# Kernel optimization log

Measured on AMD Instinct MI355X. Metric: run time of the kernel, lower is better.

## Reference

```python
import jax, jax.numpy as jnp
import numpy as np
import math

B, S, E, H, DFF = 4, 1024, 1024, 16, 4096
HD = E // H
EPS = 1e-8


def setup_inputs() -> dict:
    key = jax.random.key(0)
    ks = jax.random.split(key, 16)
    sc = 0.02
    inp = {
        'x': jax.random.normal(ks[0], (B, S, E), jnp.float32),
        'mask': jax.random.randint(ks[1], (B, S, S), 0, 2, jnp.int32),
        'Wq': jax.random.normal(ks[2], (E, E), jnp.float32) * sc,
        'bq': jnp.zeros((E,), jnp.float32),
        'Wk': jax.random.normal(ks[3], (E, E), jnp.float32) * sc,
        'bk': jnp.zeros((E,), jnp.float32),
        'Wv': jax.random.normal(ks[4], (E, E), jnp.float32) * sc,
        'bv': jnp.zeros((E,), jnp.float32),
        'Wo': jax.random.normal(ks[5], (E, E), jnp.float32) * sc,
        'bo': jnp.zeros((E,), jnp.float32),
        'W1': jax.random.normal(ks[6], (DFF, E), jnp.float32) * sc,
        'b1': jnp.zeros((DFF,), jnp.float32),
        'W2': jax.random.normal(ks[7], (E, DFF), jnp.float32) * sc,
        'b2': jnp.zeros((E,), jnp.float32),
        'g1': jnp.ones((E,), jnp.float32),
        'be1': jnp.zeros((E,), jnp.float32),
        'g2': jnp.ones((E,), jnp.float32),
        'be2': jnp.zeros((E,), jnp.float32),
    }
    return inp


def _layernorm(x, g, b):
    # torch LayerNorm here: (x-mean)/(std+eps), std is unbiased (ddof=1)
    mean = jnp.mean(x, axis=-1, keepdims=True)
    std = jnp.std(x, axis=-1, keepdims=True, ddof=1)
    return g * (x - mean) / (std + EPS) + b


def _gelu(x):
    c = math.sqrt(2.0 / math.pi)
    return 0.5 * x * (1.0 + jnp.tanh(c * (x + 0.044715 * x ** 3)))


def _block(x, mask_f, Wq, bq, Wk, bk, Wv, bv, Wo, bo, W1, b1, W2, b2, g1, be1, g2, be2):
    # --- attention sublayer (pre-norm, residual) ---
    nx = _layernorm(x, g1, be1)
    q = (nx @ Wq.T + bq).reshape(B, S, H, HD).transpose(0, 2, 1, 3)  # [B,H,S,D]
    k = (nx @ Wk.T + bk).reshape(B, S, H, HD).transpose(0, 2, 1, 3)
    v = (nx @ Wv.T + bv).reshape(B, S, H, HD).transpose(0, 2, 1, 3)
    scores = jnp.einsum('bhqd,bhkd->bhqk', q, k) / math.sqrt(HD)
    m = mask_f[:, None, :, :]  # [B,1,S,S]
    scores = jnp.where(m == 0, jnp.float32(-0.01), scores * m)
    p = jax.nn.softmax(scores, axis=-1)
    o = jnp.einsum('bhqk,bhkd->bhqd', p, v)  # [B,H,S,D]
    o = o.transpose(0, 2, 1, 3).reshape(B, S, E)
    x = x + (o @ Wo.T + bo)
    # --- FFN sublayer ---
    nx2 = _layernorm(x, g2, be2)
    ff = _gelu(nx2 @ W1.T + b1) @ W2.T + b2
    return x + ff


def reference(x, mask, Wq, bq, Wk, bk, Wv, bv, Wo, bo, W1, b1, W2, b2, g1, be1, g2, be2):
    mask_f = mask.astype(jnp.float32)
    return _block(x, mask_f, Wq, bq, Wk, bk, Wv, bv, Wo, bo, W1, b1, W2, b2, g1, be1, g2, be2)
```

## Files before the change

### kernel.cpp

```cpp
#include <hip/hip_runtime.h>
#include <math.h>

typedef __attribute__((ext_vector_type(8))) short short8;
typedef __attribute__((ext_vector_type(4))) float f32x4;
typedef __attribute__((ext_vector_type(4))) int   i32x4v;

#define B_   4
#define S_   1024
#define E_   1024
#define H_   16
#define DFF_ 4096

#define HB_MAX 4.0f

__device__ __forceinline__ ushort f2bf(float f){
  unsigned int x = __float_as_uint(f);
  x += 0x7fffu + ((x >> 16) & 1u);
  return (ushort)(x >> 16);
}

__device__ __forceinline__ unsigned int pk_bf16_trunc(float a, float b){
  return __builtin_amdgcn_perm(__float_as_uint(b), __float_as_uint(a), 0x07060302u);
}

__device__ __forceinline__ float gelu_f(float x){
  const float c = 0.7978845608028654f;
  float u = 2.0f * c * (x + 0.044715f * x * x * x);
  return x / (1.0f + __expf(-u));
}

__device__ __forceinline__ void gl2lds16(const void* g, void* l){
  __builtin_amdgcn_global_load_lds(
      (const __attribute__((address_space(1))) void*)g,
      (__attribute__((address_space(3))) void*)l, 16, 0, 0);
}

__device__ __forceinline__ int q8(float x, float s){
  float v = fmaxf(fminf(x * s, 127.f), -127.f);
  return ((int)__builtin_rintf(v)) & 255;
}
__device__ __forceinline__ int pk_i8x4(float a, float b, float c, float d, float s){
  return q8(a,s) | (q8(b,s) << 8) | (q8(c,s) << 16) | (q8(d,s) << 24);
}

__global__ __launch_bounds__(256) void prep_kernel(
    const float* __restrict__ Wq, const float* __restrict__ Wk,
    const float* __restrict__ Wv, const float* __restrict__ Wo,
    const float* __restrict__ W1, const float* __restrict__ W2,
    const float* __restrict__ bq, const float* __restrict__ bk,
    const float* __restrict__ bv, const int* __restrict__ mask,
    unsigned char* __restrict__ bQKV8, float* __restrict__ sQKV,
    unsigned char* __restrict__ bWo8, float* __restrict__ sWo,
    unsigned char* __restrict__ bW18, float* __restrict__ sW1,
    unsigned char* __restrict__ bW28, float* __restrict__ sW2,
    float* __restrict__ cbias, unsigned long long* __restrict__ maskp)
{
  int blk = blockIdx.x, t = threadIdx.x;
  int w = t >> 6, ln = t & 63;

  if (blk < 2048){
    int row = blk * 4 + w;
    const float* src; unsigned char* dst; float* sdst;
    if (row < 1024){      src = Wq + (size_t)row * 1024;
                          dst = bQKV8 + (size_t)row * 1024; sdst = sQKV + row; }
    else if (row < 2048){ src = Wk + (size_t)(row - 1024) * 1024;
                          dst = bQKV8 + (size_t)row * 1024; sdst = sQKV + row; }
    else if (row < 3072){ src = Wv + (size_t)(row - 2048) * 1024;
                          dst = bQKV8 + (size_t)row * 1024; sdst = sQKV + row; }
    else if (row < 4096){ int r = row - 3072; src = Wo + (size_t)r * 1024;
                          dst = bWo8 + (size_t)r * 1024; sdst = sWo + r; }
    else                { int r = row - 4096; src = W1 + (size_t)r * 1024;
                          dst = bW18 + (size_t)r * 1024; sdst = sW1 + r; }
    float4 v[4]; float m = 0.f;
    #pragma unroll
    for (int i = 0; i < 4; i++){
      v[i] = ((const float4*)src)[ln + i * 64];
      m = fmaxf(m, fmaxf(fmaxf(fabsf(v[i].x), fabsf(v[i].y)),
                         fmaxf(fabsf(v[i].z), fabsf(v[i].w))));
    }
    #pragma unroll
    for (int o = 32; o; o >>= 1) m = fmaxf(m, __shfl_xor(m, o));
    float mx = m + 1e-20f, qs = 127.0f / mx;
    #pragma unroll
    for (int i = 0; i < 4; i++)
      ((int*)dst)[ln + i * 64] = pk_i8x4(v[i].x, v[i].y, v[i].z, v[i].w, qs);
    if (ln == 0) *sdst = mx * (1.0f / 127.0f);
    return;
  }
  if (blk < 2304){
    int r = (blk - 2048) * 4 + w;
    const float* src = W2 + (size_t)r * 4096;
    float4 v[16]; float m = 0.f;
    #pragma unroll
    for (int i = 0; i < 16; i++){
      v[i] = ((const float4*)src)[ln + i * 64];
      m = fmaxf(m, fmaxf(fmaxf(fabsf(v[i].x), fabsf(v[i].y)),
                         fmaxf(fabsf(v[i].z), fabsf(v[i].w))));
    }
    #pragma unroll
    for (int o = 32; o; o >>= 1) m = fmaxf(m, __shfl_xor(m, o));
    float mx = m + 1e-20f, qs = 127.0f / mx;
    #pragma unroll
    for (int i = 0; i < 16; i++)
      ((int*)(bW28 + (size_t)r * 4096))[ln + i * 64] =
          pk_i8x4(v[i].x, v[i].y, v[i].z, v[i].w, qs);
    if (ln == 0) sW2[r] = mx * (1.0f / 127.0f);
    return;
  }
  if (blk == 2304){
    #pragma unroll
    for (int r = 0; r < 12; r++){
      int idx = r * 256 + t;
      cbias[idx] = (idx < 1024) ? bq[idx] : (idx < 2048 ? bk[idx - 1024] : bv[idx - 2048]);
    }
    return;
  }
  int wbase = (blk - 2305) * 16 + w * 4;
  #pragma unroll
  for (int j = 0; j < 4; j++){
    int widx = wbase + j;
    int mv = mask[(size_t)widx * 64 + ln];
    unsigned long long bal = __ballot(mv != 0);
    if (ln == 0) maskp[widx] = bal;
  }
}

__global__ __launch_bounds__(256) void ln_i8(const float* __restrict__ x,
    const float* __restrict__ g, const float* __restrict__ be,
    unsigned char* __restrict__ out8, float* __restrict__ sOut){
  int row = blockIdx.x, t = threadIdx.x;
  float4 v = ((const float4*)(x + (size_t)row * E_))[t];
  float s = v.x + v.y + v.z + v.w;
  float q = v.x*v.x + v.y*v.y + v.z*v.z + v.w*v.w;
  #pragma unroll
  for (int o = 32; o; o >>= 1){ s += __shfl_xor(s, o); q += __shfl_xor(q, o); }
  __shared__ float ss[4], sq[4], sm[4];
  int w = t >> 6;
  if ((t & 63) == 0){ ss[w] = s; sq[w] = q; }
  __syncthreads();
  s = ss[0] + ss[1] + ss[2] + ss[3];
  q = sq[0] + sq[1] + sq[2] + sq[3];
  float mean = s * (1.0f / E_);
  float var  = fmaxf((q - (float)E_ * mean * mean) * (1.0f / (E_ - 1)), 0.0f);
  float inv = 1.0f / (sqrtf(var) + 1e-8f);
  float4 gv = ((const float4*)g)[t];
  float4 bv = ((const float4*)be)[t];
  float n0 = gv.x * (v.x - mean) * inv + bv.x;
  float n1 = gv.y * (v.y - mean) * inv + bv.y;
  float n2 = gv.z * (v.z - mean) * inv + bv.z;
  float n3 = gv.w * (v.w - mean) * inv + bv.w;
  float m = fmaxf(fmaxf(fabsf(n0), fabsf(n1)), fmaxf(fabsf(n2), fabsf(n3)));
  #pragma unroll
  for (int o = 32; o; o >>= 1) m = fmaxf(m, __shfl_xor(m, o));
  if ((t & 63) == 0) sm[w] = m;
  __syncthreads();
  float mx = fmaxf(fmaxf(sm[0], sm[1]), fmaxf(sm[2], sm[3])) + 1e-20f;
  float qs = 127.0f / mx;
  ((int*)(out8 + (size_t)row * E_))[t] = pk_i8x4(n0, n1, n2, n3, qs);
  if (t == 0) sOut[row] = mx * (1.0f / 127.0f);
}

__global__ __launch_bounds__(256) void ln2_fuse(const float* __restrict__ x,
    const float* __restrict__ P, const float* __restrict__ bo,
    const float* __restrict__ g, const float* __restrict__ be,
    float* __restrict__ x2, unsigned char* __restrict__ nx28, float* __restrict__ sOut){
  int row = blockIdx.x, t = threadIdx.x;
  size_t idx = (size_t)row * 256 + t;
  float4 v  = ((const float4*)x)[idx];
  float4 p0 = ((const float4*)P)[idx];
  float4 p1 = ((const float4*)P)[idx + 1048576];
  float4 bv0 = ((const float4*)bo)[t];
  v.x += p0.x + p1.x + bv0.x;
  v.y += p0.y + p1.y + bv0.y;
  v.z += p0.z + p1.z + bv0.z;
  v.w += p0.w + p1.w + bv0.w;
  ((float4*)x2)[idx] = v;
  float s = v.x + v.y + v.z + v.w;
  float q = v.x*v.x + v.y*v.y + v.z*v.z + v.w*v.w;
  #pragma unroll
  for (int o = 32; o; o >>= 1){ s += __shfl_xor(s, o); q += __shfl_xor(q, o); }
  __shared__ float ss[4], sq[4], sm[4];
  int w = t >> 6;
  if ((t & 63) == 0){ ss[w] = s; sq[w] = q; }
  __syncthreads();
  s = ss[0] + ss[1] + ss[2] + ss[3];
  q = sq[0] + sq[1] + sq[2] + sq[3];
  float mean = s * (1.0f / E_);
  float var  = fmaxf((q - (float)E_ * mean * mean) * (1.0f / (E_ - 1)), 0.0f);
  float inv = 1.0f / (sqrtf(var) + 1e-8f);
  float4 gv = ((const float4*)g)[t];
  float4 bev = ((const float4*)be)[t];
  float n0 = gv.x * (v.x - mean) * inv + bev.x;
  float n1 = gv.y * (v.y - mean) * inv + bev.y;
  float n2 = gv.z * (v.z - mean) * inv + bev.z;
  float n3 = gv.w * (v.w - mean) * inv + bev.w;
  float m = fmaxf(fmaxf(fabsf(n0), fabsf(n1)), fmaxf(fabsf(n2), fabsf(n3)));
  #pragma unroll
  for (int o = 32; o; o >>= 1) m = fmaxf(m, __shfl_xor(m, o));
  if ((t & 63) == 0) sm[w] = m;
  __syncthreads();
  float mx = fmaxf(fmaxf(sm[0], sm[1]), fmaxf(sm[2], sm[3])) + 1e-20f;
  float qs = 127.0f / mx;
  ((int*)(nx28 + (size_t)row * E_))[t] = pk_i8x4(n0, n1, n2, n3, qs);
  if (t == 0) sOut[row] = mx * (1.0f / 127.0f);
}

__global__ __launch_bounds__(256) void reduce_out(const float* __restrict__ x2,
    const float* __restrict__ P, const float* __restrict__ b2, float* __restrict__ out){
  size_t i = (size_t)blockIdx.x * 256 + threadIdx.x;
  int col4 = i & 255;
  float4 v  = ((const float4*)x2)[i];
  float4 p0 = ((const float4*)P)[i];
  float4 p1 = ((const float4*)P)[i + 1048576];
  float4 bv = ((const float4*)b2)[col4];
  float4 o;
  o.x = v.x + p0.x + p1.x + bv.x;
  o.y = v.y + p0.y + p1.y + bv.y;
  o.z = v.z + p0.z + p1.z + bv.z;
  o.w = v.w + p0.w + p1.w + bv.w;
  ((float4*)out)[i] = o;
}

template<int MODE>
__global__ __launch_bounds__(256) void gemm_i8(
    const unsigned char* __restrict__ A8, const unsigned char* __restrict__ B8,
    const float* __restrict__ sA, const float* __restrict__ sB,
    const float* __restrict__ bias,
    ushort* __restrict__ Cb, unsigned char* __restrict__ C8, float* __restrict__ Pf,
    int K, int ldc)
{
  __shared__ __align__(16) unsigned char As[128 * 128];
  __shared__ __align__(16) unsigned char Bs[128 * 128];
  const int t = threadIdx.x, w = t >> 6, ln = t & 63;
  const int quad = ln >> 4, lc = ln & 15;
  const int wm = w >> 1, wn = w & 1;
  const int m0 = blockIdx.y * 128, n0 = blockIdx.x * 128;
  int kbeg = 0, kend = K;
  if (MODE == 2){
    int kh = K >> 1;
    kbeg = blockIdx.z * kh; kend = kbeg + kh;
    Pf += (size_t)blockIdx.z * (4096 * 1024);
  }

  i32x4v acc[4][4];
  #pragma unroll
  for (int i = 0; i < 4; i++)
    #pragma unroll
    for (int j = 0; j < 4; j++) acc[i][j] = i32x4v{0, 0, 0, 0};

  for (int k0 = kbeg; k0 < kend; k0 += 128){
    __syncthreads();
    #pragma unroll
    for (int r2 = 0; r2 < 4; r2++){
      int chunk = r2 * 256 + t;
      int row = chunk >> 3;
      int co = ((chunk & 7) ^ (row & 7)) * 16;
      gl2lds16(A8 + (size_t)(m0 + row) * K + k0 + co, As + (size_t)(r2*256 + (t & 192)) * 16);
      gl2lds16(B8 + (size_t)(n0 + row) * K + k0 + co, Bs + (size_t)(r2*256 + (t & 192)) * 16);
    }
    __syncthreads();
    #pragma unroll
    for (int kk = 0; kk < 128; kk += 64){
      const int cb = kk >> 4;
      i32x4v af[4], bfr[4];
      #pragma unroll
      for (int i = 0; i < 4; i++){
        int row = wm*64 + i*16 + lc;
        af[i]  = *(const i32x4v*)(As + (size_t)row * 128 + (((cb + quad) ^ (row & 7)) * 16));
      }
      #pragma unroll
      for (int j = 0; j < 4; j++){
        int row = wn*64 + j*16 + lc;
        bfr[j] = *(const i32x4v*)(Bs + (size_t)row * 128 + (((cb + quad) ^ (row & 7)) * 16));
      }
      #pragma unroll
      for (int i = 0; i < 4; i++)
        #pragma unroll
        for (int j = 0; j < 4; j++)
          acc[i][j] = __builtin_amdgcn_mfma_i32_16x16x64_i8(af[i], bfr[j], acc[i][j], 0, 0, 0);
    }
  }

  #pragma unroll
  for (int j = 0; j < 4; j++){
    int col = n0 + wn*64 + j*16 + lc;
    float sb = sB[col];
    float bc = (MODE == 2) ? 0.f : bias[col];
    #pragma unroll
    for (int i = 0; i < 4; i++){
      int row0 = m0 + wm*64 + i*16 + quad*4;
      #pragma unroll
      for (int r = 0; r < 4; r++){
        int row = row0 + r;
        if (MODE == 0){
          float v = (float)acc[i][j][r] * sA[row] * sb + bc;
          float sc = (col < 1024) ? 0.125f : 1.0f;
          Cb[(size_t)row * ldc + col] = f2bf(v * sc);
        } else if (MODE == 1){
          float v = gelu_f((float)acc[i][j][r] * sA[row] * sb + bc);
          C8[(size_t)row * 4096 + col] = (unsigned char)q8(v, 127.0f / HB_MAX);
        } else {
          Pf[(size_t)row * 1024 + col] = (float)acc[i][j][r] * (HB_MAX / 127.0f) * sb;
        }
      }
    }
  }
}

__global__ __launch_bounds__(256) void vT_kernel(const ushort* __restrict__ QKV,
                                                 ushort* __restrict__ Vt){
  __shared__ ushort tile[64][68];
  int st = blockIdx.x;
  int bh = blockIdx.y;
  int b = bh >> 4, h = bh & 15;
  int t = threadIdx.x;
  #pragma unroll
  for (int it = 0; it < 4; it++){
    int idx = it * 256 + t;
    int r = idx >> 4, c4 = (idx & 15) * 4;
    ushort4 v = *(const ushort4*)(QKV + ((size_t)(b*1024 + st*64 + r)) * 3072 + 2048 + h*64 + c4);
    *(ushort4*)(&tile[r][c4]) = v;
  }
  __syncthreads();
  #pragma unroll
  for (int it = 0; it < 4; it++){
    int idx = it * 256 + t;
    int d = idx >> 4, s4 = (idx & 15) * 4;
    ushort4 o;
    o.x = tile[s4+0][d]; o.y = tile[s4+1][d]; o.z = tile[s4+2][d]; o.w = tile[s4+3][d];
    *(ushort4*)(Vt + ((size_t)bh * 64 + d) * 1024 + st*64 + s4) = o;
  }
}

__global__ __launch_bounds__(256) void attn_kernel(
    const ushort* __restrict__ QKV, const ushort* __restrict__ Vt,
    const unsigned long long* __restrict__ maskp, unsigned char* __restrict__ O8)
{
  __shared__ __align__(16) ushort Ks[2][64 * 64];
  __shared__ __align__(16) ushort Vs[2][64 * 64];
  __shared__ __align__(16) ushort Ps[4][16 * 72];

  const int t = threadIdx.x, w = t >> 6, ln = t & 63;
  const int quad = ln >> 4, lc = ln & 15;
  const int bh = blockIdx.x, b = bh >> 4;
  const int q0 = blockIdx.y * 64;
  const int coff = (bh & 15) * 64;
  const size_t rb = (size_t)b * S_;

  const int myq = q0 + w*16 + lc;
  const ushort* qrow = QKV + (rb + myq) * 3072 + coff;
  short8 qf0 = *(const short8*)(qrow + quad*8);
  short8 qf1 = *(const short8*)(qrow + 32 + quad*8);
  const unsigned long long* mrow = maskp + (rb + myq) * 16;

  auto stage = [&](int kt, int buf){
    int k0 = kt * 64;
    #pragma unroll
    for (int it = 0; it < 2; it++){
      int chunk = it * 256 + t;
      int row = chunk >> 3;
      int co = ((chunk & 7) ^ (row & 7)) * 8;
      gl2lds16(QKV + (rb + k0 + row) * 3072 + 1024 + coff + co,
               Ks[buf] + (size_t)(it*256 + (t & 192)) * 8);
      gl2lds16(Vt + ((size_t)bh * 64 + row) * 1024 + k0 + co,
               Vs[buf] + (size_t)(it*256 + (t & 192)) * 8);
    }
  };

  f32x4 of[4];
  #pragma unroll
  for (int gd = 0; gd < 4; gd++) of[gd] = f32x4{0.f, 0.f, 0.f, 0.f};
  float lsum = 0.0f;
  const float PM = 0.99004983f;

  stage(0, 0);
  for (int kt = 0; kt < 16; kt++){
    int buf = kt & 1;
    unsigned long long m64 = mrow[kt];
    __syncthreads();
    if (kt < 15) stage(kt + 1, buf ^ 1);
    const ushort* ks = Ks[buf];
    const ushort* vs = Vs[buf];

    f32x4 sf[4];
    #pragma unroll
    for (int g = 0; g < 4; g++){
      int krow = g*16 + lc;
      short8 kf0 = *(const short8*)(ks + krow*64 + ((quad       ^ (lc & 7)) * 8));
      short8 kf1 = *(const short8*)(ks + krow*64 + (((4 + quad) ^ (lc & 7)) * 8));
      f32x4 z = f32x4{0.f, 0.f, 0.f, 0.f};
      z = __builtin_amdgcn_mfma_f32_16x16x32_bf16(kf0, qf0, z, 0, 0, 0);
      z = __builtin_amdgcn_mfma_f32_16x16x32_bf16(kf1, qf1, z, 0, 0, 0);
      sf[g] = z;
    }

    #pragma unroll
    for (int g = 0; g < 4; g++){
      unsigned int b4 = (unsigned int)(m64 >> (g*16 + quad*4)) & 0xFu;
      float p0 = (b4 & 1u) ? __expf(sf[g][0]) : PM;
      float p1 = (b4 & 2u) ? __expf(sf[g][1]) : PM;
      float p2 = (b4 & 4u) ? __expf(sf[g][2]) : PM;
      float p3 = (b4 & 8u) ? __expf(sf[g][3]) : PM;
      lsum += p0 + p1 + p2 + p3;
      uint2 pw;
      pw.x = pk_bf16_trunc(p0, p1);
      pw.y = pk_bf16_trunc(p2, p3);
      *(uint2*)(&Ps[w][lc*72 + g*16 + quad*4]) = pw;
    }

    short8 pf0 = *(const short8*)(&Ps[w][lc*72 + quad*8]);
    short8 pf1 = *(const short8*)(&Ps[w][lc*72 + 32 + quad*8]);
    #pragma unroll
    for (int gd = 0; gd < 4; gd++){
      int vrow = gd*16 + lc;
      short8 vf0 = *(const short8*)(vs + vrow*64 + ((quad       ^ (lc & 7)) * 8));
      short8 vf1 = *(const short8*)(vs + vrow*64 + (((4 + quad) ^ (lc & 7)) * 8));
      of[gd] = __builtin_amdgcn_mfma_f32_16x16x32_bf16(vf0, pf0, of[gd], 0, 0, 0);
      of[gd] = __builtin_amdgcn_mfma_f32_16x16x32_bf16(vf1, pf1, of[gd], 0, 0, 0);
    }
  }

  lsum += __shfl_xor(lsum, 16);
  lsum += __shfl_xor(lsum, 32);
  float inv = 1.0f / lsum;

  unsigned char* orow = O8 + (rb + myq) * E_ + coff;
  #pragma unroll
  for (int gd = 0; gd < 4; gd++){
    int pk = pk_i8x4(of[gd][0] * inv, of[gd][1] * inv,
                     of[gd][2] * inv, of[gd][3] * inv, 127.0f / HB_MAX);
    *(int*)(orow + gd*16 + quad*4) = pk;
  }
}

extern "C" void kernel_launch(void* const* d_in, const int* in_sizes, int n_in,
                              void* d_out, int out_size, void* d_ws, size_t ws_size,
                              hipStream_t stream)
{
  const float* x   = (const float*)d_in[0];
  const int*   mask= (const int*)  d_in[1];
  const float* Wq  = (const float*)d_in[2];
  const float* bq  = (const float*)d_in[3];
  const float* Wk  = (const float*)d_in[4];
  const float* bk  = (const float*)d_in[5];
  const float* Wv  = (const float*)d_in[6];
  const float* bv  = (const float*)d_in[7];
  const float* Wo  = (const float*)d_in[8];
  const float* bo  = (const float*)d_in[9];
  const float* W1  = (const float*)d_in[10];
  const float* b1  = (const float*)d_in[11];
  const float* W2  = (const float*)d_in[12];
  const float* b2  = (const float*)d_in[13];
  const float* g1  = (const float*)d_in[14];
  const float* be1 = (const float*)d_in[15];
  const float* g2  = (const float*)d_in[16];
  const float* be2 = (const float*)d_in[17];
  float* out = (float*)d_out;

  char* ws = (char*)d_ws;
  size_t off = 0;
  auto alloc = [&](size_t bytes) -> void* {
    void* p = ws + off; off += (bytes + 255) & ~(size_t)255; return p;
  };
  const size_t MM = 1024 * 1024;
  unsigned char* bQKV8 = (unsigned char*)alloc(3 * MM);
  float* sQKV  = (float*)alloc(3072 * 4);
  unsigned char* bWo8 = (unsigned char*)alloc(MM);
  float* sWo   = (float*)alloc(1024 * 4);
  unsigned char* bW18 = (unsigned char*)alloc(4 * MM);
  float* sW1   = (float*)alloc(4096 * 4);
  unsigned char* bW28 = (unsigned char*)alloc(4 * MM);
  float* sW2   = (float*)alloc(1024 * 4);
  float* cbias = (float*)alloc(3072 * 4);
  unsigned long long* maskp = (unsigned long long*)alloc(65536 * 8);
  unsigned char* nx8  = (unsigned char*)alloc(4 * MM);
  float* sX1   = (float*)alloc(4096 * 4);
  ushort* QKV  = (ushort*)alloc(12 * MM * 2);
  ushort* VtG  = (ushort*)alloc(4 * MM * 2);
  unsigned char* Ob8 = (unsigned char*)alloc(4 * MM);
  float*  x2   = (float*) alloc(4 * MM * 4);
  unsigned char* nx28 = (unsigned char*)alloc(4 * MM);
  float* sX2   = (float*)alloc(4096 * 4);
  unsigned char* hb8  = (unsigned char*)alloc(16 * MM);

  float* Pbuf = (float*)nx8;

  prep_kernel<<<6401, 256, 0, stream>>>(Wq, Wk, Wv, Wo, W1, W2, bq, bk, bv, mask,
                                        bQKV8, sQKV, bWo8, sWo, bW18, sW1, bW28, sW2,
                                        cbias, maskp);

  ln_i8<<<4096, 256, 0, stream>>>(x, g1, be1, nx8, sX1);

  gemm_i8<0><<<dim3(24, 32), 256, 0, stream>>>(
      nx8, bQKV8, sX1, sQKV, cbias, QKV, nullptr, nullptr, 1024, 3072);

  vT_kernel<<<dim3(16, 64), 256, 0, stream>>>(QKV, VtG);

  attn_kernel<<<dim3(64, 16), 256, 0, stream>>>(QKV, VtG, maskp, Ob8);

  gemm_i8<2><<<dim3(8, 32, 2), 256, 0, stream>>>(
      Ob8, bWo8, nullptr, sWo, nullptr, nullptr, nullptr, Pbuf, 1024, 1024);

  ln2_fuse<<<4096, 256, 0, stream>>>(x, Pbuf, bo, g2, be2, x2, nx28, sX2);

  gemm_i8<1><<<dim3(32, 32), 256, 0, stream>>>(
      nx28, bW18, sX2, sW1, b1, nullptr, hb8, nullptr, 1024, 4096);

  gemm_i8<2><<<dim3(8, 32, 2), 256, 0, stream>>>(
      hb8, bW28, nullptr, sW2, nullptr, nullptr, nullptr, Pbuf, 4096, 1024);

  reduce_out<<<4096, 256, 0, stream>>>(x2, Pbuf, b2, out);
}
```

Before: 316.8 us.

## Use 256x256 double-buffered int8 GEMM with XCD-aware tile remap

Replaces the 128x128 single-buffered int8 GEMM with a 256x256 tile, 512-thread kernel that double-buffers LDS and prefetches the next K slice while MFMAs run on the current one. Block indices are remapped across the 8 XCDs for better L2 locality, and s_setprio is raised around the MFMA bursts. The goal is more reuse per loaded byte and hiding global-load latency. In exchange it uses 128KB of LDS, more accumulator registers, and fewer blocks; the 1024-wide GEMMs get only 128 blocks, which may underfill the 256 CUs.

```diff
diff --git a/kernel.cpp b/kernel.cpp
--- a/kernel.cpp
+++ b/kernel.cpp
@@ -222,85 +222,155 @@
 }
 
 template<int MODE>
-__global__ __launch_bounds__(256) void gemm_i8(
+__global__ __launch_bounds__(512) void gemm256_i8(
     const unsigned char* __restrict__ A8, const unsigned char* __restrict__ B8,
     const float* __restrict__ sA, const float* __restrict__ sB,
     const float* __restrict__ bias,
     ushort* __restrict__ Cb, unsigned char* __restrict__ C8, float* __restrict__ Pf,
     int K, int ldc)
 {
-  __shared__ __align__(16) unsigned char As[128 * 128];
-  __shared__ __align__(16) unsigned char Bs[128 * 128];
+  __shared__ __align__(16) unsigned char smem[2][2][32768];
   const int t = threadIdx.x, w = t >> 6, ln = t & 63;
   const int quad = ln >> 4, lc = ln & 15;
-  const int wm = w >> 1, wn = w & 1;
-  const int m0 = blockIdx.y * 128, n0 = blockIdx.x * 128;
-  int kbeg = 0, kend = K;
+  const int wm = w >> 2, wn = w & 3;
+
+  const int gx = gridDim.x;
+  const int nwg = gx * gridDim.y;
+  int f = blockIdx.y * gx + blockIdx.x;
+  f = (f & 7) * (nwg >> 3) + (f >> 3);
+  const int n0 = (f % gx) * 256;
+  const int m0 = (f / gx) * 256;
+
+  int kbeg = 0, nT = K >> 7;
   if (MODE == 2){
     int kh = K >> 1;
-    kbeg = blockIdx.z * kh; kend = kbeg + kh;
+    kbeg = blockIdx.z * kh;
+    nT = kh >> 7;
     Pf += (size_t)blockIdx.z * (4096 * 1024);
   }
 
-  i32x4v acc[4][4];
-  #pragma unroll
-  for (int i = 0; i < 4; i++)
-    #pragma unroll
-    for (int j = 0; j < 4; j++) acc[i][j] = i32x4v{0, 0, 0, 0};
-
-  for (int k0 = kbeg; k0 < kend; k0 += 128){
-    __syncthreads();
-    #pragma unroll
-    for (int r2 = 0; r2 < 4; r2++){
-      int chunk = r2 * 256 + t;
+  auto stage_half = [&](const unsigned char* g, unsigned char* l){
+    #pragma unroll
+    for (int rr = 0; rr < 2; rr++){
+      int chunk = rr * 512 + t;
       int row = chunk >> 3;
       int co = ((chunk & 7) ^ (row & 7)) * 16;
-      gl2lds16(A8 + (size_t)(m0 + row) * K + k0 + co, As + (size_t)(r2*256 + (t & 192)) * 16);
-      gl2lds16(B8 + (size_t)(n0 + row) * K + k0 + co, Bs + (size_t)(r2*256 + (t & 192)) * 16);
-    }
-    __syncthreads();
-    #pragma unroll
-    for (int kk = 0; kk < 128; kk += 64){
-      const int cb = kk >> 4;
-      i32x4v af[4], bfr[4];
+      gl2lds16(g + (size_t)row * K + co, l + (size_t)(rr * 512 + (t & 448)) * 16);
+    }
+  };
+
+  const unsigned char* gA = A8 + (size_t)m0 * K + kbeg;
+  const unsigned char* gB = B8 + (size_t)n0 * K + kbeg;
+
+  i32x4v acc[8][4];
+  #pragma unroll
+  for (int i = 0; i < 8; i++)
+    #pragma unroll
+    for (int j = 0; j < 4; j++) acc[i][j] = i32x4v{0, 0, 0, 0};
+
+  stage_half(gA,                    &smem[0][0][0]);
+  stage_half(gA + (size_t)128 * K,  &smem[0][0][0] + 16384);
+  stage_half(gB,                    &smem[0][1][0]);
+  stage_half(gB + (size_t)128 * K,  &smem[0][1][0] + 16384);
+  asm volatile("s_waitcnt vmcnt(0)" ::: "memory");
+  __builtin_amdgcn_s_barrier();
+  asm volatile("" ::: "memory");
+
+  for (int tk = 0; tk < nT; tk++){
+    const int c = tk & 1;
+    const unsigned char* Ab = &smem[c][0][0];
+    const unsigned char* Bb = &smem[c][1][0];
+    unsigned char* As1 = &smem[c ^ 1][0][0];
+    unsigned char* Bs1 = &smem[c ^ 1][1][0];
+    const bool pre = (tk + 1 < nT);
+    const unsigned char* gAn = gA + (size_t)(tk + 1) * 128;
+    const unsigned char* gBn = gB + (size_t)(tk + 1) * 128;
+
+    #pragma unroll
+    for (int p = 0; p < 4; p++){
+      const int mh = p >> 1, nh = p & 1;
+      if (p == 0 && pre){
+        stage_half(gAn,                   As1);
+        stage_half(gAn + (size_t)128 * K, As1 + 16384);
+      }
+      if (p == 1 && pre){
+        stage_half(gBn,                   Bs1);
+        stage_half(gBn + (size_t)128 * K, Bs1 + 16384);
+      }
+      i32x4v af[4][2], bfr[2][2];
       #pragma unroll
       for (int i = 0; i < 4; i++){
-        int row = wm*64 + i*16 + lc;
-        af[i]  = *(const i32x4v*)(As + (size_t)row * 128 + (((cb + quad) ^ (row & 7)) * 16));
+        int row = wm * 128 + (mh * 4 + i) * 16 + lc;
+        int sw = row & 7;
+        af[i][0] = *(const i32x4v*)(Ab + (size_t)row * 128 + (((0 + quad) ^ sw) * 16));
+        af[i][1] = *(const i32x4v*)(Ab + (size_t)row * 128 + (((4 + quad) ^ sw) * 16));
       }
       #pragma unroll
-      for (int j = 0; j < 4; j++){
-        int row = wn*64 + j*16 + lc;
-        bfr[j] = *(const i32x4v*)(Bs + (size_t)row * 128 + (((cb + quad) ^ (row & 7)) * 16));
-      }
+      for (int j = 0; j < 2; j++){
+        int row = wn * 64 + (nh * 2 + j) * 16 + lc;
+        int sw = row & 7;
+        bfr[j][0] = *(const i32x4v*)(Bb + (size_t)row * 128 + (((0 + quad) ^ sw) * 16));
+        bfr[j][1] = *(const i32x4v*)(Bb + (size_t)row * 128 + (((4 + quad) ^ sw) * 16));
+      }
+      __builtin_amdgcn_s_barrier();
+      asm volatile("s_waitcnt lgkmcnt(0)" ::: "memory");
+      __builtin_amdgcn_s_setprio(1);
       #pragma unroll
-      for (int i = 0; i < 4; i++)
+      for (int kk2 = 0; kk2 < 2; kk2++)
         #pragma unroll
-        for (int j = 0; j < 4; j++)
-          acc[i][j] = __builtin_amdgcn_mfma_i32_16x16x64_i8(af[i], bfr[j], acc[i][j], 0, 0, 0);
-    }
-  }
-
-  #pragma unroll
-  for (int j = 0; j < 4; j++){
-    int col = n0 + wn*64 + j*16 + lc;
-    float sb = sB[col];
-    float bc = (MODE == 2) ? 0.f : bias[col];
-    #pragma unroll
-    for (int i = 0; i < 4; i++){
-      int row0 = m0 + wm*64 + i*16 + quad*4;
+        for (int i = 0; i < 4; i++)
+          #pragma unroll
+          for (int j = 0; j < 2; j++)
+            acc[mh * 4 + i][nh * 2 + j] = __builtin_amdgcn_mfma_i32_16x16x64_i8(
+                af[i][kk2], bfr[j][kk2], acc[mh * 4 + i][nh * 2 + j], 0, 0, 0);
+      __builtin_amdgcn_s_setprio(0);
+      if (p == 3){
+        asm volatile("s_waitcnt vmcnt(0)" ::: "memory");
+      }
+      __builtin_amdgcn_s_barrier();
+      if (p == 3) asm volatile("" ::: "memory");
+    }
+  }
+
+  if (MODE == 2){
+    #pragma unroll
+    for (int j = 0; j < 4; j++){
+      int col = n0 + wn * 64 + j * 16 + lc;
+      float sb = sB[col] * (HB_MAX / 127.0f);
+      #pragma unroll
+      for (int i = 0; i < 8; i++){
+        int row0 = m0 + wm * 128 + i * 16 + quad * 4;
+        #pragma unroll
+        for (int r = 0; r < 4; r++)
+          Pf[(size_t)(row0 + r) * 1024 + col] = (float)acc[i][j][r] * sb;
+      }
+    }
+  } else {
+    float sbv[4], bcv[4], scv[4];
+    int colv[4];
+    #pragma unroll
+    for (int j = 0; j < 4; j++){
+      int col = n0 + wn * 64 + j * 16 + lc;
+      colv[j] = col;
+      sbv[j] = sB[col];
+      bcv[j] = bias[col];
+      scv[j] = (MODE == 0 && col < 1024) ? 0.125f : 1.0f;
+    }
+    #pragma unroll
+    for (int i = 0; i < 8; i++){
       #pragma unroll
       for (int r = 0; r < 4; r++){
-        int row = row0 + r;
-        if (MODE == 0){
-          float v = (float)acc[i][j][r] * sA[row] * sb + bc;
-          float sc = (col < 1024) ? 0.125f : 1.0f;
-          Cb[(size_t)row * ldc + col] = f2bf(v * sc);
-        } else if (MODE == 1){
-          float v = gelu_f((float)acc[i][j][r] * sA[row] * sb + bc);
-          C8[(size_t)row * 4096 + col] = (unsigned char)q8(v, 127.0f / HB_MAX);
-        } else {
-          Pf[(size_t)row * 1024 + col] = (float)acc[i][j][r] * (HB_MAX / 127.0f) * sb;
+        int row = m0 + wm * 128 + i * 16 + quad * 4 + r;
+        float sa = sA[row];
+        #pragma unroll
+        for (int j = 0; j < 4; j++){
+          float v = (float)acc[i][j][r] * sa * sbv[j] + bcv[j];
+          if (MODE == 0){
+            Cb[(size_t)row * ldc + colv[j]] = f2bf(v * scv[j]);
+          } else {
+            C8[(size_t)row * 4096 + colv[j]] =
+                (unsigned char)q8(gelu_f(v), 127.0f / HB_MAX);
+          }
         }
       }
     }
@@ -491,22 +561,22 @@
 
   ln_i8<<<4096, 256, 0, stream>>>(x, g1, be1, nx8, sX1);
 
-  gemm_i8<0><<<dim3(24, 32), 256, 0, stream>>>(
+  gemm256_i8<0><<<dim3(12, 16), 512, 0, stream>>>(
       nx8, bQKV8, sX1, sQKV, cbias, QKV, nullptr, nullptr, 1024, 3072);
 
   vT_kernel<<<dim3(16, 64), 256, 0, stream>>>(QKV, VtG);
 
   attn_kernel<<<dim3(64, 16), 256, 0, stream>>>(QKV, VtG, maskp, Ob8);
 
-  gemm_i8<2><<<dim3(8, 32, 2), 256, 0, stream>>>(
+  gemm256_i8<2><<<dim3(4, 16, 2), 512, 0, stream>>>(
       Ob8, bWo8, nullptr, sWo, nullptr, nullptr, nullptr, Pbuf, 1024, 1024);
 
   ln2_fuse<<<4096, 256, 0, stream>>>(x, Pbuf, bo, g2, be2, x2, nx28, sX2);
 
-  gemm_i8<1><<<dim3(32, 32), 256, 0, stream>>>(
+  gemm256_i8<1><<<dim3(16, 16), 512, 0, stream>>>(
       nx28, bW18, sX2, sW1, b1, nullptr, hb8, nullptr, 1024, 4096);
 
-  gemm_i8<2><<<dim3(8, 32, 2), 256, 0, stream>>>(
+  gemm256_i8<2><<<dim3(4, 16, 2), 512, 0, stream>>>(
       hb8, bW28, nullptr, sW2, nullptr, nullptr, nullptr, Pbuf, 4096, 1024);
 
   reduce_out<<<4096, 256, 0, stream>>>(x2, Pbuf, b2, out);
```

After: 329.8 us. 1.04x slower.
